# Kernel tuning notes

Measured on AMD Instinct MI355X. Metric: run time of the kernel, lower is better.

Reference implementation:

```python
import jax, jax.numpy as jnp
from jax import lax
import numpy as np

B, T, Hh, Ww, I, D, L, N = 32, 12, 64, 128, 8, 512, 6, 16
V = I + 1          # auto + I covariates
HSZ = V            # min(D, I+1) hidden size of flattened GRN


def layer_norm(x, s, b, eps=1e-5):
    mu = jnp.mean(x, -1, keepdims=True)
    var = jnp.mean((x - mu) ** 2, -1, keepdims=True)
    return (x - mu) / jnp.sqrt(var + eps) * s + b


def interp1d(x, out_size):
    # F.interpolate(mode='linear', align_corners=True) over last axis
    n = x.shape[-1]
    pos = jnp.arange(out_size, dtype=x.dtype) * ((n - 1) / (out_size - 1))
    lo = jnp.floor(pos).astype(jnp.int32)
    hi = jnp.minimum(lo + 1, n - 1)
    frac = pos - lo.astype(x.dtype)
    return x[..., lo] * (1.0 - frac) + x[..., hi] * frac


def pconv(x, m, w, b, stride):
    # NVIDIA-style partial conv, single-channel mask, VALID padding
    kh, kw = w.shape[-2], w.shape[-1]
    dn = ('NCHW', 'OIHW', 'NCHW')
    summ = lax.conv_general_dilated(m, jnp.ones((1, 1, kh, kw), x.dtype), stride, 'VALID', dimension_numbers=dn)
    ratio = (kh * kw) / (summ + 1e-8)
    upd = jnp.clip(summ, 0.0, 1.0)
    ratio = ratio * upd
    raw = lax.conv_general_dilated(x * m, w, stride, 'VALID', dimension_numbers=dn)
    return (raw * ratio + b[None, :, None, None]) * upd, upd


def lstm_last(x, wih, whh, bih, bhh):
    # torch nn.LSTM (1 layer, batch_first), zero init state; return last hidden
    d = whh.shape[1]
    def step(carry, xt):
        h, c = carry
        g = xt @ wih.T + bih + h @ whh.T + bhh
        i, f, gg, o = jnp.split(g, 4, -1)
        c = jax.nn.sigmoid(f) * c + jax.nn.sigmoid(i) * jnp.tanh(gg)
        h = jax.nn.sigmoid(o) * jnp.tanh(c)
        return (h, c), None
    z = jnp.zeros((x.shape[0], d), x.dtype)
    (h, _), _ = lax.scan(step, (z, z), jnp.swapaxes(x, 0, 1))
    return h


def varsel(xin, rn_gate, rn_scale, rn_bias, fc1_w, fc1_b, fc2_w, fc2_b,
           glu_w, glu_b, grn_ln_s, grn_ln_b, rs_gate, rs_scale, rs_bias):
    # pytorch_forecasting VariableSelectionNetwork, all inputs pre-embedded (flag=True)
    # xin: [..., V, D]
    v = layer_norm(xin * (2.0 * jax.nn.sigmoid(rn_gate)), rn_scale, rn_bias)  # per-var ResampleNorm
    flat = xin.reshape(xin.shape[:-2] + (V * D,))
    # flattened GRN (residual=False): residual = ResampleNorm(flat -> V)
    res = layer_norm(interp1d(flat, V) * (2.0 * jax.nn.sigmoid(rs_gate)), rs_scale, rs_bias)
    h = jax.nn.elu(flat @ fc1_w.T + fc1_b)
    h = h @ fc2_w.T + fc2_b
    g = h @ glu_w.T + glu_b
    a, gb = jnp.split(g, 2, -1)
    wgt = jax.nn.softmax(layer_norm(a * jax.nn.sigmoid(gb) + res, grn_ln_s, grn_ln_b), -1)  # [..., V]
    return jnp.einsum('...vd,...v->...d', v, wgt), wgt


def reference(Xauto, Xcov, Xstatic, xmask,
              conv1_w, conv1_b, conv2_w, conv2_b, conv3_w, conv3_b,
              cov_w, static_w,
              rn_gate, rn_scale, rn_bias,
              fc1_w, fc1_b, fc2_w, fc2_b, glu_w, glu_b, grn_ln_s, grn_ln_b,
              rs_gate, rs_scale, rs_bias,
              ln1_s, ln1_b, ln2_s, ln2_b, ln3_s, ln3_b,
              lstm_wih, lstm_whh, lstm_bih, lstm_bhh,
              head_w, head_b):
    vsn = (rn_gate, rn_scale, rn_bias, fc1_w, fc1_b, fc2_w, fc2_b,
           glu_w, glu_b, grn_ln_s, grn_ln_b, rs_gate, rs_scale, rs_bias)
    # static embedding for shifts -T+1..L  -> [B, T+L, D]
    Xs = jnp.stack([jnp.roll(Xstatic, s, axis=1) for s in range(-T + 1, L + 1)], 1)
    Xs = Xs @ static_w.T
    Xs_lag, Xs_lead = Xs[:, :T], Xs[:, T:]
    # partial-conv auto embedding, all timesteps folded into batch
    m0 = xmask[0:1]
    x = Xauto.reshape(B * T, 1, Hh, Ww)
    h1, m1 = pconv(x, m0, conv1_w, conv1_b, (2, 2))
    h2, m2 = pconv(h1, m1, conv2_w, conv2_b, (2, 2))
    h3, _ = pconv(h2, m2, conv3_w, conv3_b, (Hh // 4, Ww // 4))  # [B*T, D, 1, 1]
    Xauto_emb = h3.reshape(B, T, D)
    Xcov_emb = jnp.einsum('bti,id->btid', Xcov, cov_w)           # Linear(1,D) per covariate
    Xemb = jnp.concatenate([Xauto_emb[:, :, None], Xcov_emb], 2)  # [B,T,V,D]
    Xsel, w_all = varsel(Xemb + Xs_lag[:, :, None], *vsn)        # [B,T,D], [B,T,V]
    wgts = [w_all[:, -1]]
    Xcur = layer_norm(Xsel, ln1_s, ln1_b)                        # [B,T,D]
    cov_last = Xcov_emb[:, -1]                                   # [B,I,D]
    yemb = []
    for l in range(L):
        h = lstm_last(Xcur, lstm_wih, lstm_whh, lstm_bih, lstm_bhh)
        ydec = layer_norm(h, ln2_s, ln2_b) + Xs_lead[:, l]
        yemb.append(ydec)
        if l < L - 1:
            xin2 = jnp.concatenate([ydec[:, None], cov_last], 1) + Xs_lead[:, l][:, None]
            xout, w = varsel(xin2, *vsn)
            wgts.append(w)
            Xcur = layer_norm(xout, ln3_s, ln3_b)[:, None]
    yemb = jnp.stack(yemb, 1)                                    # [B,L,D]
    Y = (yemb @ head_w.T + head_b).reshape(B, L, N, Hh, Ww)
    return Y, jnp.stack(wgts, 1)


def setup_inputs():
    key = jax.random.key(0)
    ks = jax.random.split(key, 16)
    f32 = jnp.float32
    def nrm(k, shape): return jax.random.normal(k, shape, f32) * 0.02
    return dict(
        Xauto=jax.random.normal(ks[0], (B, T, Hh, Ww), f32),
        Xcov=jax.random.normal(ks[1], (B, T, I), f32),
        Xstatic=jax.random.normal(ks[2], (B, 12), f32),
        xmask=jax.random.uniform(ks[3], (B, 1, Hh, Ww), dtype=f32),
        conv1_w=nrm(ks[4], (D // 4, 1, 2, 2)), conv1_b=jnp.zeros((D // 4,), f32),
        conv2_w=nrm(ks[5], (D // 2, D // 4, 2, 2)), conv2_b=jnp.zeros((D // 2,), f32),
        conv3_w=nrm(ks[6], (D, D // 2, Hh // 4, Ww // 4)), conv3_b=jnp.zeros((D,), f32),
        cov_w=nrm(ks[7], (I, D)),
        static_w=nrm(ks[8], (D, 12)),
        rn_gate=jnp.zeros((V, D), f32), rn_scale=jnp.ones((V, D), f32), rn_bias=jnp.zeros((V, D), f32),
        fc1_w=nrm(ks[9], (HSZ, V * D)), fc1_b=jnp.zeros((HSZ,), f32),
        fc2_w=nrm(ks[10], (HSZ, HSZ)), fc2_b=jnp.zeros((HSZ,), f32),
        glu_w=nrm(ks[11], (2 * V, HSZ)), glu_b=jnp.zeros((2 * V,), f32),
        grn_ln_s=jnp.ones((V,), f32), grn_ln_b=jnp.zeros((V,), f32),
        rs_gate=jnp.zeros((V,), f32), rs_scale=jnp.ones((V,), f32), rs_bias=jnp.zeros((V,), f32),
        ln1_s=jnp.ones((D,), f32), ln1_b=jnp.zeros((D,), f32),
        ln2_s=jnp.ones((D,), f32), ln2_b=jnp.zeros((D,), f32),
        ln3_s=jnp.ones((D,), f32), ln3_b=jnp.zeros((D,), f32),
        lstm_wih=nrm(ks[12], (4 * D, D)), lstm_whh=nrm(ks[13], (4 * D, D)),
        lstm_bih=jnp.zeros((4 * D,), f32), lstm_bhh=jnp.zeros((4 * D,), f32),
        head_w=nrm(ks[14], (N * Hh * Ww, D)), head_b=jnp.zeros((N * Hh * Ww,), f32),
    )
```

## Files before the change

### kernel.cpp

```cpp
#include <hip/hip_runtime.h>
#include <hip/hip_bf16.h>

#define DEV __device__ __forceinline__

namespace {
constexpr size_t WS_XS   = 8192;
constexpr size_t WS_H3   = WS_XS + 294912;
constexpr size_t WS_XCUR = WS_H3 + 196608;
constexpr size_t WS_XPROJ= WS_XCUR + 196608;
constexpr size_t WS_HB0  = WS_XPROJ + 786432;
constexpr size_t WS_HB1  = WS_HB0 + 16384;
constexpr size_t WS_CB   = WS_HB1 + 16384;
constexpr size_t WS_YDEC = WS_CB + 16384;
constexpr size_t WS_YEMBB= WS_YDEC + 16384;
constexpr size_t WS_GB   = WS_YEMBB + 49152;
constexpr size_t WS_XC1  = WS_GB + 65536;
constexpr size_t WS_W12  = WS_XC1 + 16384;
constexpr size_t WS_ENDF = WS_W12 + 8192;
constexpr size_t A2_BYTES = 100663296ull;
constexpr int YN = 25165824;
}

typedef __bf16 b16x8 __attribute__((ext_vector_type(8)));
typedef float  f32x4 __attribute__((ext_vector_type(4)));

DEV float sigm(float x){ return 1.f/(1.f+expf(-x)); }

DEV unsigned short f2b(float x){ __hip_bfloat16 h=__float2bfloat16(x); return *reinterpret_cast<unsigned short*>(&h); }

DEV void gload16(const unsigned short* g, unsigned short* l){
  __builtin_amdgcn_global_load_lds((const __attribute__((address_space(1))) void*)g,
                                   (__attribute__((address_space(3))) void*)l, 16, 0, 0);
}

DEV float blockReduceSum256(float v, float* red){
  const int tid = threadIdx.x;
  red[tid]=v; __syncthreads();
  #pragma unroll
  for(int s=128;s>0;s>>=1){ if(tid<s) red[tid]+=red[tid+s]; __syncthreads(); }
  const float r = red[0]; __syncthreads();
  return r;
}

__global__ __launch_bounds__(256) void k_mask(const float* __restrict__ xmask, float* __restrict__ ws){
  float* R1  = ws;
  float* U1S = ws+2048;
  float* R2  = ws+4096;
  float* U2S = ws+4608;
  float* SC  = ws+5120;
  float* RU  = ws+5632;
  __shared__ float u1[2048];
  __shared__ float u2[512];
  __shared__ float red[256];
  const int tid=threadIdx.x;
  for(int idx=tid; idx<2048; idx+=256){
    const int y=idx>>6, x=idx&63;
    const float s = xmask[(2*y)*128+2*x]+xmask[(2*y)*128+2*x+1]
                  + xmask[(2*y+1)*128+2*x]+xmask[(2*y+1)*128+2*x+1];
    const float u = fminf(fmaxf(s,0.f),1.f);
    const float r = 4.f/(s+1e-8f)*u;
    R1[idx]=r; U1S[idx]=u*u; RU[idx]=r*u*u; u1[idx]=u;
  }
  __syncthreads();
  for(int idx=tid; idx<512; idx+=256){
    const int y=idx>>5, x=idx&31;
    const float s = u1[(2*y)*64+2*x]+u1[(2*y)*64+2*x+1]+u1[(2*y+1)*64+2*x]+u1[(2*y+1)*64+2*x+1];
    const float u=fminf(fmaxf(s,0.f),1.f);
    R2[idx]=4.f/(s+1e-8f)*u; U2S[idx]=u*u; u2[idx]=u;
  }
  __syncthreads();
  float p=0; for(int idx=tid; idx<512; idx+=256) p+=u2[idx];
  const float s3 = blockReduceSum256(p,red);
  if(tid==0){ const float u=fminf(fmaxf(s3,0.f),1.f); SC[0]=512.f/(s3+1e-8f)*u; SC[1]=u; }
}

__global__ __launch_bounds__(256) void k_xs(const float* __restrict__ Xstat, const float* __restrict__ static_w, float* __restrict__ XS){
  const int gid = blockIdx.x*256+threadIdx.x;
  if(gid >= 32*18*512) return;
  const int d = gid&511, row = gid>>9;
  const int b = row/18, si = row - b*18;
  const int s = si-11;
  float acc=0.f;
  #pragma unroll
  for(int j=0;j<12;j++){
    int idx = j - s; idx %= 12; if(idx<0) idx+=12;
    acc = fmaf(Xstat[b*12+idx], static_w[d*12+j], acc);
  }
  XS[gid]=acc;
}

__global__ __launch_bounds__(256) void k_w12(const float* __restrict__ c1w, const float* __restrict__ c1b,
                                             const float* __restrict__ c2w,
                                             float* __restrict__ W12, float* __restrict__ WB){
  const int oc=threadIdx.x;
  float acc[16]={}; float accb[4]={};
  for(int ic=0;ic<128;ic++){
    const float4 w2=*(const float4*)&c2w[oc*512+ic*4];
    const float4 w1=*(const float4*)&c1w[ic*4];
    const float b1=c1b[ic];
    const float w2a[4]={w2.x,w2.y,w2.z,w2.w};
    const float w1a[4]={w1.x,w1.y,w1.z,w1.w};
    #pragma unroll
    for(int dydx=0;dydx<4;dydx++){
      const int dy=dydx>>1, dx=dydx&1;
      #pragma unroll
      for(int uv=0;uv<4;uv++){
        const int u=uv>>1, v=uv&1;
        acc[(2*dy+u)*4 + (2*dx+v)] = fmaf(w2a[dydx], w1a[uv], acc[(2*dy+u)*4+(2*dx+v)]);
      }
      accb[dydx] = fmaf(w2a[dydx], b1, accb[dydx]);
    }
  }
  #pragma unroll
  for(int t=0;t<16;t++) W12[oc*16+t]=acc[t];
  #pragma unroll
  for(int t=0;t<4;t++) WB[oc*4+t]=accb[t];
}

__global__ __launch_bounds__(256) void k_conv12(const float* __restrict__ Xauto, const float* __restrict__ xmask,
                                                const float* __restrict__ wsm,
                                                const float* __restrict__ W12, const float* __restrict__ WB,
                                                const float* __restrict__ c2b,
                                                unsigned short* __restrict__ A2){
  const int img=blockIdx.x, tid=threadIdx.x;
  __shared__ float S[64][132];
  __shared__ float u1s[2048];
  __shared__ float w12[4096];
  __shared__ float wb4[1024];
  __shared__ float r2s[512], u2s[512], cb[256];
  for(int i=tid;i<8192;i+=256){
    const int Y=i>>7, X=i&127;
    S[Y][X] = Xauto[(size_t)img*8192 + i] * xmask[i] * wsm[5632 + (Y>>1)*64 + (X>>1)];
  }
  for(int i=tid;i<2048;i+=256) u1s[i]=wsm[2048+i];
  for(int i=tid;i<4096;i+=256) w12[i]=W12[i];
  for(int i=tid;i<1024;i+=256) wb4[i]=WB[i];
  for(int i=tid;i<512;i+=256){ r2s[i]=wsm[4096+i]; u2s[i]=wsm[4608+i]; }
  if(tid<256) cb[tid]=c2b[tid];
  __syncthreads();
  float s16[2][16], us4[2][4], r2[2], u2[2];
  #pragma unroll
  for(int half=0;half<2;half++){
    const int p=tid+half*256;
    const int y2=p>>5, x2=p&31;
    #pragma unroll
    for(int ty=0;ty<4;ty++){
      const float4 v=*(const float4*)&S[4*y2+ty][4*x2];
      s16[half][ty*4+0]=v.x; s16[half][ty*4+1]=v.y; s16[half][ty*4+2]=v.z; s16[half][ty*4+3]=v.w;
    }
    #pragma unroll
    for(int dd=0;dd<4;dd++)
      us4[half][dd]=u1s[(2*y2+(dd>>1))*64 + (2*x2+(dd&1))];
    r2[half]=r2s[p]; u2[half]=u2s[p];
  }
  for(int oc=0;oc<256;oc++){
    const float4 w0=*(const float4*)&w12[oc*16];
    const float4 w1=*(const float4*)&w12[oc*16+4];
    const float4 w2=*(const float4*)&w12[oc*16+8];
    const float4 w3=*(const float4*)&w12[oc*16+12];
    const float4 wb=*(const float4*)&wb4[oc*4];
    const float cbo=cb[oc];
    #pragma unroll
    for(int half=0;half<2;half++){
      const float* s=s16[half];
      float a =  w0.x*s[0]+w0.y*s[1]+w0.z*s[2]+w0.w*s[3];
      a = fmaf(w1.x,s[4],fmaf(w1.y,s[5],fmaf(w1.z,s[6],fmaf(w1.w,s[7],a))));
      a = fmaf(w2.x,s[8],fmaf(w2.y,s[9],fmaf(w2.z,s[10],fmaf(w2.w,s[11],a))));
      a = fmaf(w3.x,s[12],fmaf(w3.y,s[13],fmaf(w3.z,s[14],fmaf(w3.w,s[15],a))));
      a += wb.x*us4[half][0]+wb.y*us4[half][1]+wb.z*us4[half][2]+wb.w*us4[half][3];
      const float v=(a*r2[half]+cbo)*u2[half];
      A2[(size_t)img*131072 + oc*512 + tid + half*256] = f2b(v);
    }
  }
}

template<int MODE, int BM, int BN, int NT>
__global__ __launch_bounds__(NT) void k_mfma(const unsigned short* __restrict__ Aq,
                                             const float* __restrict__ Bq,
                                             float* __restrict__ Cp,
                                             const float* __restrict__ bias0){
  constexpr int BK=64, CH=8;
  constexpr int NWN=2, NWM=(NT/64)/NWN;
  constexpr int RW=BM/NWM, CW=BN/NWN;
  constexpr int FM=RW/16, FN=CW/16;
  constexpr int NA=BM*CH/NT, NB=BN*CH/NT;
  constexpr int ABYTES=2*BM*BK*2, BBYTES=2*BN*BK*2;
  constexpr int CP=BN+4;
  constexpr int CSB=RW*CP*4;
  constexpr int SMB=(ABYTES+BBYTES>CSB)?(ABYTES+BBYTES):CSB;
  __shared__ __align__(16) char smem[SMB];
  unsigned short* lA=(unsigned short*)smem;
  unsigned short* lB=(unsigned short*)(smem+ABYTES);
  const int tid=threadIdx.x, lane=tid&63;
  const int w=tid>>6, wn=w&1, wm=w>>1;
  const int m0=blockIdx.y*BM, n0=blockIdx.x*BN;
  constexpr size_t lda=(MODE==1)?131072:512;
  constexpr size_t ldb=(MODE==1)?131072:512;
  int kbeg=0, kend=512;
  if constexpr(MODE==1){ kbeg=blockIdx.z*2048; kend=kbeg+2048; }

  f32x4 acc[FM][FN];
  #pragma unroll
  for(int i=0;i<FM;i++)
    #pragma unroll
    for(int j=0;j<FN;j++) acc[i][j]=f32x4{0.f,0.f,0.f,0.f};

  float4 bufB[NB][2];
  auto stageA=[&](int k0, int buf){
    #pragma unroll
    for(int i=0;i<NA;i++){
      const int c=tid+i*NT, r=c>>3, gk=c&7;
      gload16(Aq + (size_t)(m0+r)*lda + k0 + ((gk ^ (r&7))<<3),
              lA + (size_t)buf*BM*64 + c*8);
    }
  };
  auto fetchB=[&](int k0){
    #pragma unroll
    for(int i=0;i<NB;i++){
      const int c=tid+i*NT, r=c>>3, gk=c&7;
      const float* p=Bq + (size_t)(n0+r)*ldb + k0+gk*8;
      bufB[i][0]=*(const float4*)p; bufB[i][1]=*(const float4*)(p+4);
    }
  };
  auto commitB=[&](int buf){
    #pragma unroll
    for(int i=0;i<NB;i++){
      const int c=tid+i*NT, r=c>>3, gk=c&7;
      union { unsigned short us[8]; int4 q; } u;
      const float4 a=bufB[i][0], b=bufB[i][1];
      u.us[0]=f2b(a.x); u.us[1]=f2b(a.y); u.us[2]=f2b(a.z); u.us[3]=f2b(a.w);
      u.us[4]=f2b(b.x); u.us[5]=f2b(b.y); u.us[6]=f2b(b.z); u.us[7]=f2b(b.w);
      *(int4*)(lB + (size_t)buf*BN*64 + ((size_t)gk*BN + r)*8)=u.q;
    }
  };

  int cur=0;
  stageA(kbeg,0);
  fetchB(kbeg);
  commitB(0);
  __syncthreads();
  for(int k0=kbeg; k0<kend; k0+=BK){
    const bool nxt=(k0+BK<kend);
    if(nxt){ stageA(k0+BK, cur^1); fetchB(k0+BK); }
    #pragma unroll
    for(int ks=0; ks<2; ks++){
      const int gkr=ks*4+(lane>>4);
      b16x8 av[FM], bv[FN];
      #pragma unroll
      for(int i=0;i<FM;i++){
        const int row=wm*RW+i*16+(lane&15);
        av[i]=*(const b16x8*)(lA + (size_t)cur*BM*64 + row*64 + ((gkr ^ (row&7))<<3));
      }
      #pragma unroll
      for(int j=0;j<FN;j++){
        const int row=wn*CW+j*16+(lane&15);
        bv[j]=*(const b16x8*)(lB + (size_t)cur*BN*64 + ((size_t)gkr*BN + row)*8);
      }
      #pragma unroll
      for(int i=0;i<FM;i++)
        #pragma unroll
        for(int j=0;j<FN;j++)
          acc[i][j]=__builtin_amdgcn_mfma_f32_16x16x32_bf16(av[i],bv[j],acc[i][j],0,0,0);
    }
    if(nxt) commitB(cur^1);
    __syncthreads();
    cur^=1;
  }

  const int r4=(lane>>4)*4, cl=lane&15;
  float (*cs)[CP]=(float(*)[CP])smem;
  for(int ch=0; ch<NWM; ++ch){
    __syncthreads();
    if(wm==ch){
      #pragma unroll
      for(int i=0;i<FM;i++)
        #pragma unroll
        for(int j=0;j<FN;j++)
          #pragma unroll
          for(int ri=0;ri<4;ri++)
            cs[i*16+r4+ri][wn*CW+j*16+cl]=acc[i][j][ri];
    }
    __syncthreads();
    for(int idx=tid; idx<RW*(BN/4); idx+=NT){
      const int row=idx/(BN/4), q=idx%(BN/4);
      float4 v=*(float4*)&cs[row][q*4];
      const int gr=m0+ch*RW+row;
      if constexpr(MODE==1){
        *(float4*)&Cp[((size_t)blockIdx.z*384+gr)*512 + n0+q*4]=v;
      } else {
        const float4 b=*(const float4*)&bias0[n0+q*4];
        v.x+=b.x; v.y+=b.y; v.z+=b.z; v.w+=b.w;
        *(float4*)&Cp[(size_t)gr*131072 + n0+q*4]=v;
      }
    }
  }
}

__global__ __launch_bounds__(256) void k_gemm3(const float* __restrict__ Ap,
                                               const float* __restrict__ Bp,
                                               float* __restrict__ Cp,
                                               const float* __restrict__ bias0,
                                               const float* __restrict__ bias1){
  __shared__ float As[16][68];
  __shared__ float Bs[16][68];
  const int tid=threadIdx.x;
  const int m0=blockIdx.y*64, n0=blockIdx.x*64;
  float acc[4][4]={};
  const int tm=tid&15, tn=tid>>4;
  const int lrow=tid>>2, lk4=(tid&3)*4;
  for(int k0=0; k0<512; k0+=16){
    {
      const float4 t=*(const float4*)(Ap + (size_t)(m0+lrow)*512 + k0+lk4);
      As[lk4+0][lrow]=t.x; As[lk4+1][lrow]=t.y; As[lk4+2][lrow]=t.z; As[lk4+3][lrow]=t.w;
    }
    {
      const float4 t=*(const float4*)(Bp + (size_t)(n0+lrow)*512 + k0+lk4);
      Bs[lk4+0][lrow]=t.x; Bs[lk4+1][lrow]=t.y; Bs[lk4+2][lrow]=t.z; Bs[lk4+3][lrow]=t.w;
    }
    __syncthreads();
    #pragma unroll
    for(int kk=0;kk<16;kk++){
      const float4 a4=*(const float4*)&As[kk][tm*4];
      const float4 b4=*(const float4*)&Bs[kk][tn*4];
      const float av[4]={a4.x,a4.y,a4.z,a4.w};
      const float bv[4]={b4.x,b4.y,b4.z,b4.w};
      #pragma unroll
      for(int i=0;i<4;i++)
        #pragma unroll
        for(int j=0;j<4;j++)
          acc[i][j]=fmaf(av[i],bv[j],acc[i][j]);
    }
    __syncthreads();
  }
  #pragma unroll
  for(int i=0;i<4;i++){
    const int m=m0+tm*4+i;
    #pragma unroll
    for(int j=0;j<4;j++){
      const int n=n0+tn*4+j;
      Cp[(size_t)m*2048+n]=acc[i][j]+bias0[n]+bias1[n];
    }
  }
}

__global__ __launch_bounds__(256) void k_conv3red(const float* __restrict__ part, const float* __restrict__ c3b,
                                                  const float* __restrict__ wsm, float* __restrict__ h3){
  const int gid=blockIdx.x*256+threadIdx.x;
  if(gid>=196608) return;
  const int m=gid>>9, n=gid&511;
  float s=0.f;
  for(int z=0;z<64;z++) s+=part[((size_t)z*384+m)*512+n];
  h3[gid]=(s*wsm[5120]+c3b[n])*wsm[5121];
}

__global__ __launch_bounds__(256) void k_varsel(
  const float* __restrict__ v0p, const float* __restrict__ Xcov, const float* __restrict__ cov_w,
  const float* __restrict__ Xs,
  const float* __restrict__ rn_gate, const float* __restrict__ rn_scale, const float* __restrict__ rn_bias,
  const float* __restrict__ fc1_w, const float* __restrict__ fc1_b,
  const float* __restrict__ fc2_w, const float* __restrict__ fc2_b,
  const float* __restrict__ glu_w, const float* __restrict__ glu_b,
  const float* __restrict__ grn_s, const float* __restrict__ grn_b,
  const float* __restrict__ rs_gate, const float* __restrict__ rs_scale, const float* __restrict__ rs_bias,
  const float* __restrict__ lns, const float* __restrict__ lnb,
  float* __restrict__ outX, float* __restrict__ wgt_base)
{
  __shared__ float xin[9][512];
  __shared__ float hpart[256][9];
  __shared__ float red[256];
  __shared__ float obuf[512];
  __shared__ float muv[9], rsv[9], wsmx[9], hbuf9[9];
  const int tid=threadIdx.x, tk=blockIdx.x;
  const int b=tk/12, t=tk-b*12;
  const float* xs=Xs+((size_t)b*18+t)*512;
  const float* covrow=Xcov+(size_t)tk*8;
  const float* v0r=v0p+(size_t)tk*512;
  float* orow=outX+(size_t)tk*512;
  float* wp=(t==11)? wgt_base+b*54 : nullptr;
  for(int idx=tid; idx<4608; idx+=256){
    const int vv=idx>>9, d=idx&511;
    const float base=xs[d];
    xin[vv][d] = (vv==0) ? (v0r[d]+base) : fmaf(covrow[vv-1], cov_w[(vv-1)*512+d], base);
  }
  __syncthreads();
  for(int vv=0; vv<9; vv++){
    const int d0=tid*2;
    const float y0=xin[vv][d0]  *2.f*sigm(rn_gate[vv*512+d0]);
    const float y1=xin[vv][d0+1]*2.f*sigm(rn_gate[vv*512+d0+1]);
    const float mu=blockReduceSum256(y0+y1,red)*(1.f/512.f);
    const float q0=y0-mu, q1=y1-mu;
    const float var=blockReduceSum256(q0*q0+q1*q1,red)*(1.f/512.f);
    if(tid==0){ muv[vv]=mu; rsv[vv]=rsqrtf(var+1e-5f); }
  }
  {
    float hp[9]={0,0,0,0,0,0,0,0,0};
    const float* flat=&xin[0][0];
    for(int i=tid;i<4608;i+=256){
      const float f=flat[i];
      #pragma unroll
      for(int j=0;j<9;j++) hp[j]=fmaf(f, fc1_w[j*4608+i], hp[j]);
    }
    #pragma unroll
    for(int j=0;j<9;j++) hpart[tid][j]=hp[j];
  }
  __syncthreads();
  if(tid<9){
    float s=0.f;
    for(int t2=0;t2<256;t2++) s+=hpart[t2][tid];
    hbuf9[tid]=s;
  }
  __syncthreads();
  if(tid==0){
    const float* flat=&xin[0][0];
    float rg[9];
    #pragma unroll
    for(int k=0;k<9;k++){
      const float pos=(float)k*575.875f;
      const int lo=(int)floorf(pos);
      const float fr=pos-(float)lo;
      int hi=lo+1; if(hi>4607)hi=4607;
      rg[k]=(flat[lo]*(1.f-fr)+flat[hi]*fr)*2.f*sigm(rs_gate[k]);
    }
    float mu=0.f; for(int k=0;k<9;k++) mu+=rg[k]; mu*=(1.f/9.f);
    float va=0.f; for(int k=0;k<9;k++){const float dd=rg[k]-mu; va+=dd*dd;} va*=(1.f/9.f);
    float rstd=rsqrtf(va+1e-5f);
    float resv[9];
    for(int k=0;k<9;k++) resv[k]=(rg[k]-mu)*rstd*rs_scale[k]+rs_bias[k];
    float h[9];
    for(int j=0;j<9;j++){ const float x=hbuf9[j]+fc1_b[j]; h[j]=x>0.f?x:expm1f(x); }
    float h2[9];
    for(int j=0;j<9;j++){ float s=fc2_b[j]; for(int k=0;k<9;k++) s=fmaf(h[k],fc2_w[j*9+k],s); h2[j]=s; }
    float lg[9];
    for(int j=0;j<9;j++){
      float sa=glu_b[j];   for(int k=0;k<9;k++) sa=fmaf(h2[k],glu_w[j*9+k],sa);
      float sg=glu_b[9+j]; for(int k=0;k<9;k++) sg=fmaf(h2[k],glu_w[(9+j)*9+k],sg);
      lg[j]=sa*sigm(sg)+resv[j];
    }
    mu=0.f; for(int k=0;k<9;k++) mu+=lg[k]; mu*=(1.f/9.f);
    va=0.f; for(int k=0;k<9;k++){const float dd=lg[k]-mu; va+=dd*dd;} va*=(1.f/9.f);
    rstd=rsqrtf(va+1e-5f);
    float lnv[9], mx=-1e30f;
    for(int k=0;k<9;k++){ lnv[k]=(lg[k]-mu)*rstd*grn_s[k]+grn_b[k]; mx=fmaxf(mx,lnv[k]); }
    float se=0.f;
    for(int k=0;k<9;k++){ lnv[k]=expf(lnv[k]-mx); se+=lnv[k]; }
    const float inv=1.f/se;
    for(int k=0;k<9;k++){ const float w=lnv[k]*inv; wsmx[k]=w; if(wp) wp[k]=w; }
  }
  __syncthreads();
  for(int d=tid; d<512; d+=256){
    float o=0.f;
    #pragma unroll
    for(int vv=0;vv<9;vv++){
      const float g=2.f*sigm(rn_gate[vv*512+d]);
      const float y=xin[vv][d]*g;
      const float vval=(y-muv[vv])*rsv[vv]*rn_scale[vv*512+d]+rn_bias[vv*512+d];
      o=fmaf(vval,wsmx[vv],o);
    }
    obuf[d]=o;
  }
  __syncthreads();
  float p=0.f;
  for(int d=tid;d<512;d+=256) p+=obuf[d];
  const float mu2=blockReduceSum256(p,red)*(1.f/512.f);
  p=0.f;
  for(int d=tid;d<512;d+=256){const float dd=obuf[d]-mu2; p+=dd*dd;}
  const float var2=blockReduceSum256(p,red)*(1.f/512.f);
  const float rstd2=rsqrtf(var2+1e-5f);
  for(int d=tid;d<512;d+=256) orow[d]=(obuf[d]-mu2)*rstd2*lns[d]+lnb[d];
}

__global__ __launch_bounds__(256) void k_lstm_s(const float* __restrict__ xproj, const float* __restrict__ whh,
     const float* __restrict__ hr, float* __restrict__ hw, float* __restrict__ cg, int t){
  __shared__ float wlds[8][516];
  __shared__ float hlds[32][516];
  __shared__ float gv[32][9];
  const int bid=blockIdx.x, tid=threadIdx.x;
  const int j0=bid*2;
  for(int idx=tid; idx<1024; idx+=256){
    const int r2=idx>>7, k4=(idx&127)*4;
    const int gate2=r2>>1, jl2=r2&1;
    *(float4*)&wlds[r2][k4] = *(const float4*)&whh[(size_t)(gate2*512 + j0 + jl2)*512 + k4];
  }
  if(t>0){
    for(int idx=tid; idx<4096; idx+=256){
      const int rb=idx>>7, k4=(idx&127)*4;
      *(float4*)&hlds[rb][k4] = *(const float4*)&hr[rb*512+k4];
    }
  }
  __syncthreads();
  const int r=tid&7, b=tid>>3;
  const int gate=r>>1, jloc=r&1;
  float acc = xproj[((size_t)b*12+t)*2048 + gate*512 + j0 + jloc];
  if(t>0){
    float4 s={0.f,0.f,0.f,0.f};
    for(int k=0;k<512;k+=4){
      const float4 hk=*(const float4*)&hlds[b][k];
      const float4 wk=*(const float4*)&wlds[r][k];
      s.x=fmaf(hk.x,wk.x,s.x); s.y=fmaf(hk.y,wk.y,s.y);
      s.z=fmaf(hk.z,wk.z,s.z); s.w=fmaf(hk.w,wk.w,s.w);
    }
    acc+=(s.x+s.y)+(s.z+s.w);
  }
  gv[b][r]=acc;
  __syncthreads();
  if(tid<64){
    const int bb=tid>>1, jj=tid&1;
    const float gi=gv[bb][0+jj], gf=gv[bb][2+jj], gg=gv[bb][4+jj], go=gv[bb][6+jj];
    float c = (t==0) ? 0.f : cg[bb*512 + j0 + jj];
    c = sigm(gf)*c + sigm(gi)*tanhf(gg);
    cg[bb*512 + j0 + jj]=c;
    hw[bb*512 + j0 + jj]=sigm(go)*tanhf(c);
  }
}

__global__ __launch_bounds__(256) void k_declstm(const float* __restrict__ Xc1, const float* __restrict__ wih,
        const float* __restrict__ bih, const float* __restrict__ bhh, float* __restrict__ hout){
  __shared__ float xs_[32][516];
  const int n=blockIdx.x, tid=threadIdx.x;
  for(int idx=tid; idx<16384; idx+=256){
    const int bb=idx>>9, k=idx&511;
    xs_[bb][k]=Xc1[bb*512+k];
  }
  __syncthreads();
  const int jl=tid>>4, bl=tid&15;
  const int j=n*16+jl;
  const float* wi=wih+(size_t)j*512;
  const float* wg=wih+(size_t)(1024+j)*512;
  const float* wo=wih+(size_t)(1536+j)*512;
  const float bi_=bih[j]+bhh[j];
  const float bg_=bih[1024+j]+bhh[1024+j];
  const float bo_=bih[1536+j]+bhh[1536+j];
  #pragma unroll
  for(int half=0; half<2; half++){
    const int b=bl+half*16;
    float gi=bi_, gg=bg_, go=bo_;
    for(int k=0;k<512;k+=4){
      const float4 xk=*(const float4*)&xs_[b][k];
      const float4 a0=*(const float4*)(wi+k);
      const float4 a1=*(const float4*)(wg+k);
      const float4 a2=*(const float4*)(wo+k);
      gi += xk.x*a0.x+xk.y*a0.y+xk.z*a0.z+xk.w*a0.w;
      gg += xk.x*a1.x+xk.y*a1.y+xk.z*a1.z+xk.w*a1.w;
      go += xk.x*a2.x+xk.y*a2.y+xk.z*a2.z+xk.w*a2.w;
    }
    const float c=sigm(gi)*tanhf(gg);
    hout[b*512+j]=sigm(go)*tanhf(c);
  }
}

__global__ __launch_bounds__(256) void k_ydvs(
  int l,
  const float* __restrict__ hb, const float* __restrict__ Xcov, const float* __restrict__ cov_w,
  const float* __restrict__ Xs,
  const float* __restrict__ rn_gate, const float* __restrict__ rn_scale, const float* __restrict__ rn_bias,
  const float* __restrict__ fc1_w, const float* __restrict__ fc1_b,
  const float* __restrict__ fc2_w, const float* __restrict__ fc2_b,
  const float* __restrict__ glu_w, const float* __restrict__ glu_b,
  const float* __restrict__ grn_s, const float* __restrict__ grn_b,
  const float* __restrict__ rs_gate, const float* __restrict__ rs_scale, const float* __restrict__ rs_bias,
  const float* __restrict__ ln2s, const float* __restrict__ ln2b,
  const float* __restrict__ ln3s, const float* __restrict__ ln3b,
  float* __restrict__ outX, float* __restrict__ wgt_base, unsigned short* __restrict__ yembB)
{
  __shared__ float xin[9][512];
  __shared__ float hpart[256][9];
  __shared__ float red[256];
  __shared__ float obuf[512];
  __shared__ float ydl[512];
  __shared__ float muv[9], rsv[9], wsmx[9], hbuf9[9];
  const int tid=threadIdx.x, b=blockIdx.x;
  const float* xs=Xs+((size_t)b*18+12+l)*512;
  for(int d=tid;d<512;d+=256) obuf[d]=hb[b*512+d];
  __syncthreads();
  {
    float p=0.f; for(int d=tid;d<512;d+=256) p+=obuf[d];
    const float mu=blockReduceSum256(p,red)*(1.f/512.f);
    p=0.f; for(int d=tid;d<512;d+=256){const float dd=obuf[d]-mu;p+=dd*dd;}
    const float var=blockReduceSum256(p,red)*(1.f/512.f);
    const float rstd=rsqrtf(var+1e-5f);
    for(int d=tid;d<512;d+=256){
      const float o=(obuf[d]-mu)*rstd*ln2s[d]+ln2b[d]+xs[d];
      ydl[d]=o;
      yembB[((size_t)b*6+l)*512+d]=f2b(o);
    }
  }
  __syncthreads();
  if(l==5) return;
  const float* covrow=Xcov+((size_t)b*12+11)*8;
  float* orow=outX+(size_t)b*512;
  float* wp=wgt_base+b*54+(l+1)*9;
  for(int idx=tid; idx<4608; idx+=256){
    const int vv=idx>>9, d=idx&511;
    const float base=xs[d];
    xin[vv][d] = (vv==0) ? (ydl[d]+base) : fmaf(covrow[vv-1], cov_w[(vv-1)*512+d], base);
  }
  __syncthreads();
  for(int vv=0; vv<9; vv++){
    const int d0=tid*2;
    const float y0=xin[vv][d0]  *2.f*sigm(rn_gate[vv*512+d0]);
    const float y1=xin[vv][d0+1]*2.f*sigm(rn_gate[vv*512+d0+1]);
    const float mu=blockReduceSum256(y0+y1,red)*(1.f/512.f);
    const float q0=y0-mu, q1=y1-mu;
    const float var=blockReduceSum256(q0*q0+q1*q1,red)*(1.f/512.f);
    if(tid==0){ muv[vv]=mu; rsv[vv]=rsqrtf(var+1e-5f); }
  }
  {
    float hp[9]={0,0,0,0,0,0,0,0,0};
    const float* flat=&xin[0][0];
    for(int i=tid;i<4608;i+=256){
      const float f=flat[i];
      #pragma unroll
      for(int j=0;j<9;j++) hp[j]=fmaf(f, fc1_w[j*4608+i], hp[j]);
    }
    #pragma unroll
    for(int j=0;j<9;j++) hpart[tid][j]=hp[j];
  }
  __syncthreads();
  if(tid<9){
    float s=0.f;
    for(int t2=0;t2<256;t2++) s+=hpart[t2][tid];
    hbuf9[tid]=s;
  }
  __syncthreads();
  if(tid==0){
    const float* flat=&xin[0][0];
    float rg[9];
    #pragma unroll
    for(int k=0;k<9;k++){
      const float pos=(float)k*575.875f;
      const int lo=(int)floorf(pos);
      const float fr=pos-(float)lo;
      int hi=lo+1; if(hi>4607)hi=4607;
      rg[k]=(flat[lo]*(1.f-fr)+flat[hi]*fr)*2.f*sigm(rs_gate[k]);
    }
    float mu=0.f; for(int k=0;k<9;k++) mu+=rg[k]; mu*=(1.f/9.f);
    float va=0.f; for(int k=0;k<9;k++){const float dd=rg[k]-mu; va+=dd*dd;} va*=(1.f/9.f);
    float rstd=rsqrtf(va+1e-5f);
    float resv[9];
    for(int k=0;k<9;k++) resv[k]=(rg[k]-mu)*rstd*rs_scale[k]+rs_bias[k];
    float h[9];
    for(int j=0;j<9;j++){ const float x=hbuf9[j]+fc1_b[j]; h[j]=x>0.f?x:expm1f(x); }
    float h2[9];
    for(int j=0;j<9;j++){ float s=fc2_b[j]; for(int k=0;k<9;k++) s=fmaf(h[k],fc2_w[j*9+k],s); h2[j]=s; }
    float lg[9];
    for(int j=0;j<9;j++){
      float sa=glu_b[j];   for(int k=0;k<9;k++) sa=fmaf(h2[k],glu_w[j*9+k],sa);
      float sg=glu_b[9+j]; for(int k=0;k<9;k++) sg=fmaf(h2[k],glu_w[(9+j)*9+k],sg);
      lg[j]=sa*sigm(sg)+resv[j];
    }
    mu=0.f; for(int k=0;k<9;k++) mu+=lg[k]; mu*=(1.f/9.f);
    va=0.f; for(int k=0;k<9;k++){const float dd=lg[k]-mu; va+=dd*dd;} va*=(1.f/9.f);
    rstd=rsqrtf(va+1e-5f);
    float lnv[9], mx=-1e30f;
    for(int k=0;k<9;k++){ lnv[k]=(lg[k]-mu)*rstd*grn_s[k]+grn_b[k]; mx=fmaxf(mx,lnv[k]); }
    float se=0.f;
    for(int k=0;k<9;k++){ lnv[k]=expf(lnv[k]-mx); se+=lnv[k]; }
    const float inv=1.f/se;
    for(int k=0;k<9;k++){ const float w=lnv[k]*inv; wsmx[k]=w; wp[k]=w; }
  }
  __syncthreads();
  for(int d=tid; d<512; d+=256){
    float o=0.f;
    #pragma unroll
    for(int vv=0;vv<9;vv++){
      const float g=2.f*sigm(rn_gate[vv*512+d]);
      const float y=xin[vv][d]*g;
      const float vval=(y-muv[vv])*rsv[vv]*rn_scale[vv*512+d]+rn_bias[vv*512+d];
      o=fmaf(vval,wsmx[vv],o);
    }
    obuf[d]=o;
  }
  __syncthreads();
  float p=0.f;
  for(int d=tid;d<512;d+=256) p+=obuf[d];
  const float mu2=blockReduceSum256(p,red)*(1.f/512.f);
  p=0.f;
  for(int d=tid;d<512;d+=256){const float dd=obuf[d]-mu2; p+=dd*dd;}
  const float var2=blockReduceSum256(p,red)*(1.f/512.f);
  const float rstd2=rsqrtf(var2+1e-5f);
  for(int d=tid;d<512;d+=256) orow[d]=(obuf[d]-mu2)*rstd2*ln3s[d]+ln3b[d];
}

extern "C" void kernel_launch(void* const* d_in, const int* in_sizes, int n_in,
                              void* d_out, int out_size, void* d_ws, size_t ws_size,
                              hipStream_t stream){
  (void)in_sizes; (void)n_in; (void)out_size; (void)ws_size;
  const float* Xauto=(const float*)d_in[0];
  const float* Xcov =(const float*)d_in[1];
  const float* Xstat=(const float*)d_in[2];
  const float* xmask=(const float*)d_in[3];
  const float* c1w=(const float*)d_in[4];
  const float* c1b=(const float*)d_in[5];
  const float* c2w=(const float*)d_in[6];
  const float* c2b=(const float*)d_in[7];
  const float* c3w=(const float*)d_in[8];
  const float* c3b=(const float*)d_in[9];
  const float* cov_w=(const float*)d_in[10];
  const float* static_w=(const float*)d_in[11];
  const float* rn_gate=(const float*)d_in[12];
  const float* rn_scale=(const float*)d_in[13];
  const float* rn_bias=(const float*)d_in[14];
  const float* fc1_w=(const float*)d_in[15];
  const float* fc1_b=(const float*)d_in[16];
  const float* fc2_w=(const float*)d_in[17];
  const float* fc2_b=(const float*)d_in[18];
  const float* glu_w=(const float*)d_in[19];
  const float* glu_b=(const float*)d_in[20];
  const float* grn_s=(const float*)d_in[21];
  const float* grn_b=(const float*)d_in[22];
  const float* rs_gate=(const float*)d_in[23];
  const float* rs_scale=(const float*)d_in[24];
  const float* rs_bias=(const float*)d_in[25];
  const float* ln1s=(const float*)d_in[26];
  const float* ln1b=(const float*)d_in[27];
  const float* ln2s=(const float*)d_in[28];
  const float* ln2b=(const float*)d_in[29];
  const float* ln3s=(const float*)d_in[30];
  const float* ln3b=(const float*)d_in[31];
  const float* wih=(const float*)d_in[32];
  const float* whh=(const float*)d_in[33];
  const float* bih=(const float*)d_in[34];
  const float* bhh=(const float*)d_in[35];
  const float* head_w=(const float*)d_in[36];
  const float* head_b=(const float*)d_in[37];

  float* out=(float*)d_out;
  float* ws=(float*)d_ws;
  unsigned short* A2=(unsigned short*)((char*)d_ws + WS_ENDF*sizeof(float));
  float* part=(float*)((char*)d_ws + WS_ENDF*sizeof(float) + A2_BYTES);
  unsigned short* yembB=(unsigned short*)(ws+WS_YEMBB);

  const dim3 blk(256);
  k_mask<<<1,blk,0,stream>>>(xmask, ws);
  k_xs<<<1152,blk,0,stream>>>(Xstat, static_w, ws+WS_XS);
  k_w12<<<1,blk,0,stream>>>(c1w, c1b, c2w, ws+WS_W12, ws+WS_W12+4096);
  k_conv12<<<384,blk,0,stream>>>(Xauto, xmask, ws, ws+WS_W12, ws+WS_W12+4096, c2b, A2);
  k_mfma<1,384,128,512><<<dim3(4,1,64),dim3(512),0,stream>>>(A2, c3w, part, nullptr);
  k_conv3red<<<768,blk,0,stream>>>(part, c3b, ws, ws+WS_H3);
  k_varsel<<<384,blk,0,stream>>>(ws+WS_H3, Xcov, cov_w, ws+WS_XS,
      rn_gate,rn_scale,rn_bias, fc1_w,fc1_b,fc2_w,fc2_b, glu_w,glu_b, grn_s,grn_b,
      rs_gate,rs_scale,rs_bias, ln1s,ln1b, ws+WS_XCUR, out+YN);
  k_gemm3<<<dim3(32,6),blk,0,stream>>>(ws+WS_XCUR, wih, ws+WS_XPROJ, bih, bhh);
  for(int t=0;t<12;t++){
    const float* hr = ws + ((t&1) ? WS_HB1 : WS_HB0);
    float* hw = ws + ((t&1) ? WS_HB0 : WS_HB1);
    k_lstm_s<<<256,blk,0,stream>>>(ws+WS_XPROJ, whh, hr, hw, ws+WS_CB, t);
  }
  for(int l=0;l<6;l++){
    if(l>0){
      k_declstm<<<32,blk,0,stream>>>(ws+WS_XC1, wih, bih, bhh, ws+WS_HB0);
    }
    k_ydvs<<<32,blk,0,stream>>>(l, ws+WS_HB0, Xcov, cov_w, ws+WS_XS,
        rn_gate,rn_scale,rn_bias, fc1_w,fc1_b,fc2_w,fc2_b, glu_w,glu_b, grn_s,grn_b,
        rs_gate,rs_scale,rs_bias, ln2s,ln2b, ln3s,ln3b,
        ws+WS_XC1, out+YN, yembB);
  }
  k_mfma<2,192,128,512><<<dim3(1024,1),dim3(512),0,stream>>>(yembB, head_w, out, head_b);
}
```

Before: 812.2 us.

## Fuse decoder LSTM cell into per-step variable-selection kernel

Removes the separate k_declstm launch and computes the decoder LSTM cell (input projection over i,g,o gates, zero state) inside k_ydvs for steps after the first. Each of the 32 blocks now handles one batch row and computes all 512 hidden units itself, which saves five launches and an intermediate global round-trip. In exchange every block streams the full 3x512x512 input weights, so weight traffic rises 32-fold and is served mostly from cache while only 32 blocks run. An extra barrier is added before ydl is overwritten.

```diff
diff --git a/kernel.cpp b/kernel.cpp
--- a/kernel.cpp
+++ b/kernel.cpp
@@ -513,44 +513,11 @@
   }
 }
 
-__global__ __launch_bounds__(256) void k_declstm(const float* __restrict__ Xc1, const float* __restrict__ wih,
-        const float* __restrict__ bih, const float* __restrict__ bhh, float* __restrict__ hout){
-  __shared__ float xs_[32][516];
-  const int n=blockIdx.x, tid=threadIdx.x;
-  for(int idx=tid; idx<16384; idx+=256){
-    const int bb=idx>>9, k=idx&511;
-    xs_[bb][k]=Xc1[bb*512+k];
-  }
-  __syncthreads();
-  const int jl=tid>>4, bl=tid&15;
-  const int j=n*16+jl;
-  const float* wi=wih+(size_t)j*512;
-  const float* wg=wih+(size_t)(1024+j)*512;
-  const float* wo=wih+(size_t)(1536+j)*512;
-  const float bi_=bih[j]+bhh[j];
-  const float bg_=bih[1024+j]+bhh[1024+j];
-  const float bo_=bih[1536+j]+bhh[1536+j];
-  #pragma unroll
-  for(int half=0; half<2; half++){
-    const int b=bl+half*16;
-    float gi=bi_, gg=bg_, go=bo_;
-    for(int k=0;k<512;k+=4){
-      const float4 xk=*(const float4*)&xs_[b][k];
-      const float4 a0=*(const float4*)(wi+k);
-      const float4 a1=*(const float4*)(wg+k);
-      const float4 a2=*(const float4*)(wo+k);
-      gi += xk.x*a0.x+xk.y*a0.y+xk.z*a0.z+xk.w*a0.w;
-      gg += xk.x*a1.x+xk.y*a1.y+xk.z*a1.z+xk.w*a1.w;
-      go += xk.x*a2.x+xk.y*a2.y+xk.z*a2.z+xk.w*a2.w;
-    }
-    const float c=sigm(gi)*tanhf(gg);
-    hout[b*512+j]=sigm(go)*tanhf(c);
-  }
-}
-
 __global__ __launch_bounds__(256) void k_ydvs(
   int l,
-  const float* __restrict__ hb, const float* __restrict__ Xcov, const float* __restrict__ cov_w,
+  const float* __restrict__ hb, const float* __restrict__ Xc1,
+  const float* __restrict__ wih, const float* __restrict__ bih, const float* __restrict__ bhh,
+  const float* __restrict__ Xcov, const float* __restrict__ cov_w,
   const float* __restrict__ Xs,
   const float* __restrict__ rn_gate, const float* __restrict__ rn_scale, const float* __restrict__ rn_bias,
   const float* __restrict__ fc1_w, const float* __restrict__ fc1_b,
@@ -570,14 +537,42 @@
   __shared__ float muv[9], rsv[9], wsmx[9], hbuf9[9];
   const int tid=threadIdx.x, b=blockIdx.x;
   const float* xs=Xs+((size_t)b*18+12+l)*512;
-  for(int d=tid;d<512;d+=256) obuf[d]=hb[b*512+d];
-  __syncthreads();
+  if(l==0){
+    for(int d=tid;d<512;d+=256) obuf[d]=hb[b*512+d];
+    __syncthreads();
+  } else {
+    for(int d=tid;d<512;d+=256) ydl[d]=Xc1[b*512+d];
+    __syncthreads();
+    #pragma unroll
+    for(int half=0;half<2;half++){
+      const int j=tid+half*256;
+      const float* wi=wih+(size_t)j*512;
+      const float* wg=wih+(size_t)(1024+j)*512;
+      const float* wo=wih+(size_t)(1536+j)*512;
+      float gi=bih[j]+bhh[j];
+      float gg=bih[1024+j]+bhh[1024+j];
+      float go=bih[1536+j]+bhh[1536+j];
+      for(int k=0;k<512;k+=4){
+        const float4 xk=*(const float4*)&ydl[k];
+        const float4 a0=*(const float4*)(wi+k);
+        const float4 a1=*(const float4*)(wg+k);
+        const float4 a2=*(const float4*)(wo+k);
+        gi += xk.x*a0.x+xk.y*a0.y+xk.z*a0.z+xk.w*a0.w;
+        gg += xk.x*a1.x+xk.y*a1.y+xk.z*a1.z+xk.w*a1.w;
+        go += xk.x*a2.x+xk.y*a2.y+xk.z*a2.z+xk.w*a2.w;
+      }
+      const float c=sigm(gi)*tanhf(gg);
+      obuf[j]=sigm(go)*tanhf(c);
+    }
+    __syncthreads();
+  }
   {
     float p=0.f; for(int d=tid;d<512;d+=256) p+=obuf[d];
     const float mu=blockReduceSum256(p,red)*(1.f/512.f);
     p=0.f; for(int d=tid;d<512;d+=256){const float dd=obuf[d]-mu;p+=dd*dd;}
     const float var=blockReduceSum256(p,red)*(1.f/512.f);
     const float rstd=rsqrtf(var+1e-5f);
+    __syncthreads();
     for(int d=tid;d<512;d+=256){
       const float o=(obuf[d]-mu)*rstd*ln2s[d]+ln2b[d]+xs[d];
       ydl[d]=o;
@@ -747,10 +742,7 @@
     k_lstm_s<<<256,blk,0,stream>>>(ws+WS_XPROJ, whh, hr, hw, ws+WS_CB, t);
   }
   for(int l=0;l<6;l++){
-    if(l>0){
-      k_declstm<<<32,blk,0,stream>>>(ws+WS_XC1, wih, bih, bhh, ws+WS_HB0);
-    }
-    k_ydvs<<<32,blk,0,stream>>>(l, ws+WS_HB0, Xcov, cov_w, ws+WS_XS,
+    k_ydvs<<<32,blk,0,stream>>>(l, ws+WS_HB0, ws+WS_XC1, wih, bih, bhh, Xcov, cov_w, ws+WS_XS,
         rn_gate,rn_scale,rn_bias, fc1_w,fc1_b,fc2_w,fc2_b, glu_w,glu_b, grn_s,grn_b,
         rs_gate,rs_scale,rs_bias, ln2s,ln2b, ln3s,ln3b,
         ws+WS_XC1, out+YN, yembB);
```

Result: slower. 1.111 ms (+36.8%).
